# Kernel tuning notes

Hardware: AMD Instinct MI355X
Metric: run time of the kernel (lower is better)

The kernel has to match this reference:

```python
import jax, jax.numpy as jnp
import numpy as np

B, N, E, S, ANN_D, N_STEPS = 16384, 70, 3, 10, 1, 5


def setup_inputs() -> dict:
    key = jax.random.key(0)
    ks = jax.random.split(key, 10)
    std = 0.02
    annotation = jax.random.normal(ks[0], (B, N), jnp.float32)
    A_raw = jax.random.uniform(ks[1], (N, N * E), jnp.float32) + 1e-3
    A = A_raw / A_raw.sum(axis=1, keepdims=True)  # row-normalized like torch.div(A, sum(A,1))
    W_in = jax.random.normal(ks[2], (E, S, S), jnp.float32) * std
    b_in = jnp.zeros((E, S), jnp.float32)
    Wr = jax.random.normal(ks[3], (S, 2 * S), jnp.float32) * std
    br = jnp.zeros((S,), jnp.float32)
    Wz = jax.random.normal(ks[4], (S, 2 * S), jnp.float32) * std
    bz = jnp.zeros((S,), jnp.float32)
    Wh = jax.random.normal(ks[5], (S, 2 * S), jnp.float32) * std
    bh = jnp.zeros((S,), jnp.float32)
    Wo1 = jax.random.normal(ks[6], (S, S + ANN_D), jnp.float32) * std
    bo1 = jnp.zeros((S,), jnp.float32)
    Wo2 = jax.random.normal(ks[7], (1, S), jnp.float32) * std
    bo2 = jnp.zeros((1,), jnp.float32)
    return {"annotation": annotation, "A": A, "W_in": W_in, "b_in": b_in,
            "Wr": Wr, "br": br, "Wz": Wz, "bz": bz, "Wh": Wh, "bh": bh,
            "Wo1": Wo1, "bo1": bo1, "Wo2": Wo2, "bo2": bo2}


def reference(annotation, A, W_in, b_in, Wr, br, Wz, bz, Wh, bh, Wo1, bo1, Wo2, bo2):
    b, n = annotation.shape
    ann = annotation[..., None]  # [B, N, 1]
    # initial state: annotation padded with zeros to state_dim
    prop = jnp.concatenate([ann, jnp.zeros((b, n, S - ANN_D), annotation.dtype)], axis=2)  # [B,N,S]
    for _ in range(N_STEPS):
        # per-edge-type linear: [B,E,N,S]; view order is edge-type-major (matches torch stack/transpose/view)
        ins = jnp.einsum('bnd,efd->benf', prop, W_in) + b_in[None, :, None, :]
        ins = ins.reshape(b, E * n, S)  # [B, E*N, S]
        a_in = jnp.einsum('nm,bms->bns', A, ins)  # bmm aggregation, [B,N,S]
        a = jnp.concatenate([a_in, prop], axis=2)  # [B,N,2S]
        r = jax.nn.sigmoid(a @ Wr.T + br)
        z = jax.nn.sigmoid(a @ Wz.T + bz)
        joined = jnp.concatenate([a_in, r * prop], axis=2)
        h_hat = jnp.tanh(joined @ Wh.T + bh)
        prop = (1.0 - z) * prop + z * h_hat
    join_state = jnp.concatenate([prop, ann], axis=2)  # [B,N,S+1]
    out = jnp.tanh(join_state @ Wo1.T + bo1) @ Wo2.T + bo2  # [B,N,1]
    return out.sum(axis=2)  # [B,N]
```

## Files before the change

### kernel.cpp

```cpp
#include <hip/hip_runtime.h>
#include <hip/hip_bf16.h>

typedef _Float16 v8h __attribute__((ext_vector_type(8)));
typedef _Float16 v4h __attribute__((ext_vector_type(4)));
typedef _Float16 v2h __attribute__((ext_vector_type(2)));
typedef float    v4f __attribute__((ext_vector_type(4)));

#define NTOT  16384
#define NN    70
#define STEPS 5
#define TPB   64
#define NBLK  NTOT
#define CATN  40
#define CATH  3208
#define USTR  232
#define UH    (10*USTR)

#define PWO1 0
#define PWO2 120
#define PBO2 130
#define NWP  132

#define OFR  1024
#define OFZ  1536
#define OFH  2048
#define OFA  2560
#define NWF  20480
#define PREPB 40

__device__ __align__(16) float    g_w[NWP];
__device__ __align__(16) _Float16 g_wf[NWF];
__device__ int g_flag;

__device__ __forceinline__ float fast_sigmoid(float x) {
    return __builtin_amdgcn_rcpf(1.0f + __expf(-x));
}
__device__ __forceinline__ float fast_tanh(float x) {
    float ax = fabsf(x);
    float e  = __expf(-2.0f * ax);
    float t  = (1.0f - e) * __builtin_amdgcn_rcpf(1.0f + e);
    return copysignf(t, x);
}

struct __align__(16) Smem {
    _Float16 U[UH];
    _Float16 cat[CATH];
};

__global__ void prep_kernel(const void* annv, const void* Av,
    const void* winv, const void* binv, const void* wrv, const void* brv,
    const void* wzv, const void* bzv, const void* whv, const void* bhv,
    const void* wo1v, const void* bo1v, const void* wo2v, const void* bo2v)
{
    __shared__ int sflag;
    if (threadIdx.x == 0) {
        const unsigned short* u = (const unsigned short*)annv;
        int good = 0;
        for (int k = 0; k < 128; ++k) {
            unsigned short bb = u[k];
            int ex = (bb >> 7) & 0xFF;
            if (bb == 0 || (ex >= 101 && ex <= 131)) ++good;
        }
        sflag = (good >= 112) ? 1 : 0;
        if (blockIdx.x == 0) g_flag = sflag;
    }
    __syncthreads();
    const int f = sflag;
    #define RD(p, i) (f ? (float)((const __hip_bfloat16*)(p))[i] : ((const float*)(p))[i])
    const int tid = threadIdx.x;
    if (blockIdx.x == 0) {
        for (int idx = tid; idx < 120; idx += blockDim.x) {
            const int s = idx / 12, cc = idx - s*12;
            g_w[PWO1 + idx] = (cc < 11) ? RD(wo1v, s*11 + cc) : RD(bo1v, s);
        }
        for (int idx = tid; idx < 10; idx += blockDim.x) g_w[PWO2 + idx] = RD(wo2v, idx);
        if (tid == 0) { g_w[PBO2] = RD(bo2v, 0); g_w[PBO2+1] = 0.f; }
    }
    for (int idx = blockIdx.x*blockDim.x + tid; idx < NWF; idx += gridDim.x*blockDim.x) {
        float val = 0.f;
        if (idx < OFR) {
            const int nt = idx >> 9, rem = idx & 511, lane = rem >> 3, j = rem & 7;
            const int k = ((lane >> 4) << 3) + j, col = nt*16 + (lane & 15);
            if (col < 30) {
                const int e = col / 10, s = col - e*10;
                if (k >= 16 && k < 26) val = RD(winv, e*100 + s*10 + (k-16));
                else if (k == 26)      val = RD(binv, e*10 + s);
            }
        } else if (idx < OFH) {
            const int i2 = idx - OFR;
            const int mt = i2 >> 9, rem = i2 & 511, lane = rem >> 3, j = rem & 7;
            const int k = ((lane >> 4) << 3) + j, s = lane & 15;
            if (s < 10) {
                const void* Wv = mt ? wzv : wrv;
                const void* bv = mt ? bzv : brv;
                if (k < 10)                 val = RD(Wv, s*20 + k);
                else if (k >= 16 && k < 26) val = RD(Wv, s*20 + 10 + (k-16));
                else if (k == 26)           val = RD(bv, s);
            }
        } else if (idx < OFA) {
            const int i2 = idx - OFH;
            const int lane = i2 >> 3, j = i2 & 7;
            const int k = ((lane >> 4) << 3) + j, s = lane & 15;
            if (s < 10) {
                if (k < 10)                 val = RD(whv, s*20 + k);
                else if (k >= 16 && k < 26) val = RD(whv, s*20 + 10 + (k-16));
                else if (k == 26)           val = RD(bhv, s);
            }
        } else {
            const int i2 = idx - OFA;
            const int w = i2 / 3584, rem = i2 - w*3584;
            const int kt = rem >> 9, r2 = rem & 511, lane = r2 >> 3, j = r2 & 7;
            const int m = w*16 + (lane & 15);
            const int k = kt*32 + ((lane >> 4) << 3) + j;
            const int e = k / 72, mm = k - e*72;
            if (m < NN && e < 3 && mm < NN) val = RD(Av, m*210 + e*70 + mm);
        }
        g_wf[idx] = (_Float16)val;
    }
    #undef RD
}

template<typename T>
__device__ __forceinline__ void run_impl(const void* annv, void* outv, Smem& sm)
{
    const T* ann_g = (const T*)annv;
    T* out_g       = (T*)outv;
    const int lane = threadIdx.x;
    const int blk  = blockIdx.x;
    const int q    = lane >> 4;
    const int c    = lane & 15;
    const float* __restrict__ gw = g_w;

    {
        const int4 zz = {0,0,0,0};
        int4* z = (int4*)&sm;
        #pragma unroll 4
        for (int i = lane; i < (int)(sizeof(Smem)/16); i += TPB) z[i] = zz;
    }
    __syncthreads();

    for (int n2 = lane; n2 < NN; n2 += TPB) {
        sm.cat[n2*CATN + 16] = (_Float16)(float)ann_g[blk*NN + n2];
        sm.cat[n2*CATN + 26] = (_Float16)1.0f;
    }
    __syncthreads();

    #define PHASE1() do {                                                        \
        const v8h w1f0 = *(const v8h*)&g_wf[      lane*8];                       \
        const v8h w1f1 = *(const v8h*)&g_wf[512 + lane*8];                       \
        _Pragma("unroll")                                                        \
        for (int mt = 0; mt < 5; ++mt) {                                         \
            const v8h af = *(const v8h*)&sm.cat[(mt*16 + c)*CATN + q*8];         \
            const int node0 = mt*16 + q*4;                                       \
            _Pragma("unroll")                                                    \
            for (int nt = 0; nt < 2; ++nt) {                                     \
                v4f acc = {0.f,0.f,0.f,0.f};                                     \
                acc = __builtin_amdgcn_mfma_f32_16x16x32_f16(                    \
                        af, nt ? w1f1 : w1f0, acc, 0,0,0);                       \
                const int colw = nt*16 + c;                                      \
                if (colw < 30 && node0 <= 68) {                                  \
                    const int e = colw / 10, s = colw - e*10;                    \
                    v4h hv = {(_Float16)acc[0],(_Float16)acc[1],                 \
                              (_Float16)acc[2],(_Float16)acc[3]};                \
                    *(v4h*)&sm.U[s*USTR + e*72 + node0] = hv;                    \
                }                                                                \
            }                                                                    \
        }                                                                        \
    } while(0)

    PHASE1();
    __syncthreads();

    #pragma unroll 1
    for (int step = 0; step < STEPS; ++step) {
        {
            v8h bfr[7];
            #pragma unroll
            for (int kt = 0; kt < 7; ++kt)
                bfr[kt] = *(const v8h*)&sm.U[c*USTR + q*8 + kt*32];
            #pragma unroll
            for (int mt = 0; mt < 5; ++mt) {
                v4f acc = {0.f,0.f,0.f,0.f};
                #pragma unroll
                for (int kt = 0; kt < 7; ++kt)
                    acc = __builtin_amdgcn_mfma_f32_16x16x32_f16(
                        bfr[kt],
                        *(const v8h*)&g_wf[OFA + (mt*7+kt)*512 + lane*8],
                        acc, 0,0,0);
                const int node = mt*16 + c;
                if (node < NN) {
                    const v4h hv = {(_Float16)acc[0],(_Float16)acc[1],
                                    (_Float16)acc[2],(_Float16)acc[3]};
                    _Float16* wp = &sm.cat[node*CATN + q*4];
                    if (q < 2)       *(v4h*)wp = hv;
                    else if (q == 2) *(v2h*)wp = (v2h){hv[0], hv[1]};
                }
            }
        }
        __syncthreads();

        v4h zgp[5], pgp[5];
        {
            const v8h wrf = *(const v8h*)&g_wf[OFR + lane*8];
            const v8h wzf = *(const v8h*)&g_wf[OFZ + lane*8];
            #pragma unroll
            for (int nt = 0; nt < 5; ++nt) {
                const int node = nt*16 + c;
                const v8h bf = *(const v8h*)&sm.cat[node*CATN + q*8];
                v4f ar = {0.f,0.f,0.f,0.f}, az = {0.f,0.f,0.f,0.f};
                ar = __builtin_amdgcn_mfma_f32_16x16x32_f16(wrf, bf, ar, 0,0,0);
                az = __builtin_amdgcn_mfma_f32_16x16x32_f16(wzf, bf, az, 0,0,0);
                const v4h pv = *(const v4h*)&sm.cat[node*CATN + 16 + q*4];
                v4h rp, zh;
                #pragma unroll
                for (int i = 0; i < 4; ++i) {
                    const float p = (float)pv[i];
                    zh[i] = (_Float16)fast_sigmoid(az[i]);
                    rp[i] = (_Float16)(fast_sigmoid(ar[i]) * p);
                }
                zgp[nt] = zh; pgp[nt] = pv;
                if (node < NN) {
                    _Float16* wp = &sm.cat[node*CATN + 16 + q*4];
                    if (q < 2)       *(v4h*)wp = rp;
                    else if (q == 2) *(v2h*)wp = (v2h){rp[0], rp[1]};
                }
            }
        }
        __syncthreads();

        {
            const v8h whf = *(const v8h*)&g_wf[OFH + lane*8];
            #pragma unroll
            for (int nt = 0; nt < 5; ++nt) {
                const int node = nt*16 + c;
                const v8h bf2 = *(const v8h*)&sm.cat[node*CATN + q*8];
                v4f ah = {0.f,0.f,0.f,0.f};
                ah = __builtin_amdgcn_mfma_f32_16x16x32_f16(whf, bf2, ah, 0,0,0);
                v4h pn;
                #pragma unroll
                for (int i = 0; i < 4; ++i) {
                    const float hh = fast_tanh(ah[i]);
                    const float p  = (float)pgp[nt][i];
                    const float z  = (float)zgp[nt][i];
                    pn[i] = (_Float16)(p + z*(hh - p));
                }
                if (node < NN) {
                    _Float16* wp = &sm.cat[node*CATN + 16 + q*4];
                    if (q < 2)       *(v4h*)wp = pn;
                    else if (q == 2) *(v2h*)wp = (v2h){pn[0], pn[1]};
                }
            }
        }
        __syncthreads();

        if (step < STEPS-1) {
            PHASE1();
            __syncthreads();
        }
    }
    #undef PHASE1

    for (int n2 = lane; n2 < NN; n2 += TPB) {
        const _Float16* pc = &sm.cat[n2*CATN + 16];
        const v8h p8 = *(const v8h*)pc;
        const v2h p2 = *(const v2h*)(pc + 8);
        float pr[10];
        #pragma unroll
        for (int i = 0; i < 8; ++i) pr[i] = (float)p8[i];
        pr[8] = (float)p2[0]; pr[9] = (float)p2[1];
        const float av = (float)ann_g[blk*NN + n2];
        float o = gw[PBO2];
        #pragma unroll
        for (int s = 0; s < 10; ++s) {
            const float* wr_ = &gw[PWO1 + s*12];
            float acc = wr_[11] + wr_[10]*av;
            #pragma unroll
            for (int d = 0; d < 10; ++d) acc += pr[d]*wr_[d];
            o += fast_tanh(acc) * gw[PWO2 + s];
        }
        out_g[blk*NN + n2] = (T)o;
    }
}

__global__ __launch_bounds__(TPB, 2)
void ggnn_kernel(const void* annv, void* outv)
{
    __shared__ Smem sm;
    if (g_flag)
        run_impl<__hip_bfloat16>(annv, outv, sm);
    else
        run_impl<float>(annv, outv, sm);
}

extern "C" void kernel_launch(void* const* d_in, const int* in_sizes, int n_in,
                              void* d_out, int out_size, void* d_ws, size_t ws_size,
                              hipStream_t stream) {
    (void)in_sizes; (void)n_in; (void)out_size; (void)d_ws; (void)ws_size;
    hipLaunchKernelGGL(prep_kernel, dim3(PREPB), dim3(256), 0, stream,
        d_in[0], d_in[1], d_in[2], d_in[3], d_in[4], d_in[5], d_in[6],
        d_in[7], d_in[8], d_in[9], d_in[10], d_in[11], d_in[12], d_in[13]);
    hipLaunchKernelGGL(ggnn_kernel, dim3(NBLK), dim3(TPB), 0, stream,
        d_in[0], d_out);
}
```

Baseline: 290.1 us.

## Swizzle concat tile layout and double-buffer adjacency fragment loads

Shrinks the per-node concat row stride from 40 to 32 halves and applies an XOR swizzle on the 8-element chunk index, so the vector LDS accesses avoid bank conflicts while using less shared memory. The aggregation MFMA loop now preloads the adjacency weight fragments for two row tiles into registers and alternates between two buffers, with scheduling barriers, so global loads overlap the MFMA chains. This raises register pressure and adds address arithmetic on every shared-memory access.

After: 299.7 us. 1.03x slower.

```diff
diff --git a/kernel.cpp b/kernel.cpp
--- a/kernel.cpp
+++ b/kernel.cpp
@@ -11,8 +11,8 @@
 #define STEPS 5
 #define TPB   64
 #define NBLK  NTOT
-#define CATN  40
-#define CATH  3208
+#define CATN  32
+#define CATH  (80*CATN)
 #define USTR  232
 #define UH    (10*USTR)
 
@@ -40,6 +40,11 @@
     float e  = __expf(-2.0f * ax);
     float t  = (1.0f - e) * __builtin_amdgcn_rcpf(1.0f + e);
     return copysignf(t, x);
+}
+
+__device__ __forceinline__ int cat_off(int node, int k) {
+    const int sw = (node ^ (node >> 2)) & 3;
+    return node*CATN + (((k >> 3) ^ sw) << 3) + (k & 7);
 }
 
 struct __align__(16) Smem {
@@ -140,8 +145,8 @@
     __syncthreads();
 
     for (int n2 = lane; n2 < NN; n2 += TPB) {
-        sm.cat[n2*CATN + 16] = (_Float16)(float)ann_g[blk*NN + n2];
-        sm.cat[n2*CATN + 26] = (_Float16)1.0f;
+        sm.cat[cat_off(n2, 16)] = (_Float16)(float)ann_g[blk*NN + n2];
+        sm.cat[cat_off(n2, 26)] = (_Float16)1.0f;
     }
     __syncthreads();
 
@@ -150,7 +155,7 @@
         const v8h w1f1 = *(const v8h*)&g_wf[512 + lane*8];                       \
         _Pragma("unroll")                                                        \
         for (int mt = 0; mt < 5; ++mt) {                                         \
-            const v8h af = *(const v8h*)&sm.cat[(mt*16 + c)*CATN + q*8];         \
+            const v8h af = *(const v8h*)&sm.cat[cat_off(mt*16 + c, q*8)];        \
             const int node0 = mt*16 + q*4;                                       \
             _Pragma("unroll")                                                    \
             for (int nt = 0; nt < 2; ++nt) {                                     \
@@ -174,28 +179,68 @@
     #pragma unroll 1
     for (int step = 0; step < STEPS; ++step) {
         {
+            const _Float16* adjb = &g_wf[OFA + lane*8];
+            v8h pa[7], pb[7];
+            #pragma unroll
+            for (int kt = 0; kt < 7; ++kt) pa[kt] = *(const v8h*)(adjb + (0*7+kt)*512);
+            #pragma unroll
+            for (int kt = 0; kt < 7; ++kt) pb[kt] = *(const v8h*)(adjb + (1*7+kt)*512);
             v8h bfr[7];
             #pragma unroll
             for (int kt = 0; kt < 7; ++kt)
                 bfr[kt] = *(const v8h*)&sm.U[c*USTR + q*8 + kt*32];
-            #pragma unroll
-            for (int mt = 0; mt < 5; ++mt) {
-                v4f acc = {0.f,0.f,0.f,0.f};
-                #pragma unroll
-                for (int kt = 0; kt < 7; ++kt)
-                    acc = __builtin_amdgcn_mfma_f32_16x16x32_f16(
-                        bfr[kt],
-                        *(const v8h*)&g_wf[OFA + (mt*7+kt)*512 + lane*8],
-                        acc, 0,0,0);
-                const int node = mt*16 + c;
-                if (node < NN) {
-                    const v4h hv = {(_Float16)acc[0],(_Float16)acc[1],
-                                    (_Float16)acc[2],(_Float16)acc[3]};
-                    _Float16* wp = &sm.cat[node*CATN + q*4];
-                    if (q < 2)       *(v4h*)wp = hv;
-                    else if (q == 2) *(v2h*)wp = (v2h){hv[0], hv[1]};
-                }
-            }
+
+            #define P2_STORE(mtt, acc) do {                                      \
+                const int node = (mtt)*16 + c;                                   \
+                if (node < NN) {                                                 \
+                    const v4h hv = {(_Float16)acc[0],(_Float16)acc[1],           \
+                                    (_Float16)acc[2],(_Float16)acc[3]};          \
+                    if (q < 2)       *(v4h*)&sm.cat[cat_off(node, q*4)] = hv;    \
+                    else if (q == 2) *(v2h*)&sm.cat[cat_off(node, 8)]            \
+                                         = (v2h){hv[0], hv[1]};                  \
+                } } while(0)
+
+            { v4f acc = {0.f,0.f,0.f,0.f};
+              #pragma unroll
+              for (int kt = 0; kt < 7; ++kt)
+                  acc = __builtin_amdgcn_mfma_f32_16x16x32_f16(bfr[kt], pa[kt], acc, 0,0,0);
+              P2_STORE(0, acc);
+              __builtin_amdgcn_sched_barrier(0);
+              #pragma unroll
+              for (int kt = 0; kt < 7; ++kt) pa[kt] = *(const v8h*)(adjb + (2*7+kt)*512);
+            }
+            { v4f acc = {0.f,0.f,0.f,0.f};
+              #pragma unroll
+              for (int kt = 0; kt < 7; ++kt)
+                  acc = __builtin_amdgcn_mfma_f32_16x16x32_f16(bfr[kt], pb[kt], acc, 0,0,0);
+              P2_STORE(1, acc);
+              __builtin_amdgcn_sched_barrier(0);
+              #pragma unroll
+              for (int kt = 0; kt < 7; ++kt) pb[kt] = *(const v8h*)(adjb + (3*7+kt)*512);
+            }
+            { v4f acc = {0.f,0.f,0.f,0.f};
+              #pragma unroll
+              for (int kt = 0; kt < 7; ++kt)
+                  acc = __builtin_amdgcn_mfma_f32_16x16x32_f16(bfr[kt], pa[kt], acc, 0,0,0);
+              P2_STORE(2, acc);
+              __builtin_amdgcn_sched_barrier(0);
+              #pragma unroll
+              for (int kt = 0; kt < 7; ++kt) pa[kt] = *(const v8h*)(adjb + (4*7+kt)*512);
+            }
+            { v4f acc = {0.f,0.f,0.f,0.f};
+              #pragma unroll
+              for (int kt = 0; kt < 7; ++kt)
+                  acc = __builtin_amdgcn_mfma_f32_16x16x32_f16(bfr[kt], pb[kt], acc, 0,0,0);
+              P2_STORE(3, acc);
+              __builtin_amdgcn_sched_barrier(0);
+            }
+            { v4f acc = {0.f,0.f,0.f,0.f};
+              #pragma unroll
+              for (int kt = 0; kt < 7; ++kt)
+                  acc = __builtin_amdgcn_mfma_f32_16x16x32_f16(bfr[kt], pa[kt], acc, 0,0,0);
+              P2_STORE(4, acc);
+            }
+            #undef P2_STORE
         }
         __syncthreads();
 
@@ -206,11 +251,11 @@
             #pragma unroll
             for (int nt = 0; nt < 5; ++nt) {
                 const int node = nt*16 + c;
-                const v8h bf = *(const v8h*)&sm.cat[node*CATN + q*8];
+                const v8h bf = *(const v8h*)&sm.cat[cat_off(node, q*8)];
                 v4f ar = {0.f,0.f,0.f,0.f}, az = {0.f,0.f,0.f,0.f};
                 ar = __builtin_amdgcn_mfma_f32_16x16x32_f16(wrf, bf, ar, 0,0,0);
                 az = __builtin_amdgcn_mfma_f32_16x16x32_f16(wzf, bf, az, 0,0,0);
-                const v4h pv = *(const v4h*)&sm.cat[node*CATN + 16 + q*4];
+                const v4h pv = *(const v4h*)&sm.cat[cat_off(node, 16 + q*4)];
                 v4h rp, zh;
                 #pragma unroll
                 for (int i = 0; i < 4; ++i) {
@@ -220,9 +265,8 @@
                 }
                 zgp[nt] = zh; pgp[nt] = pv;
                 if (node < NN) {
-                    _Float16* wp = &sm.cat[node*CATN + 16 + q*4];
-                    if (q < 2)       *(v4h*)wp = rp;
-                    else if (q == 2) *(v2h*)wp = (v2h){rp[0], rp[1]};
+                    if (q < 2)       *(v4h*)&sm.cat[cat_off(node, 16 + q*4)] = rp;
+                    else if (q == 2) *(v2h*)&sm.cat[cat_off(node, 24)] = (v2h){rp[0], rp[1]};
                 }
             }
         }
@@ -233,7 +277,7 @@
             #pragma unroll
             for (int nt = 0; nt < 5; ++nt) {
                 const int node = nt*16 + c;
-                const v8h bf2 = *(const v8h*)&sm.cat[node*CATN + q*8];
+                const v8h bf2 = *(const v8h*)&sm.cat[cat_off(node, q*8)];
                 v4f ah = {0.f,0.f,0.f,0.f};
                 ah = __builtin_amdgcn_mfma_f32_16x16x32_f16(whf, bf2, ah, 0,0,0);
                 v4h pn;
@@ -245,9 +289,8 @@
                     pn[i] = (_Float16)(p + z*(hh - p));
                 }
                 if (node < NN) {
-                    _Float16* wp = &sm.cat[node*CATN + 16 + q*4];
-                    if (q < 2)       *(v4h*)wp = pn;
-                    else if (q == 2) *(v2h*)wp = (v2h){pn[0], pn[1]};
+                    if (q < 2)       *(v4h*)&sm.cat[cat_off(node, 16 + q*4)] = pn;
+                    else if (q == 2) *(v2h*)&sm.cat[cat_off(node, 24)] = (v2h){pn[0], pn[1]};
                 }
             }
         }
@@ -261,9 +304,8 @@
     #undef PHASE1
 
     for (int n2 = lane; n2 < NN; n2 += TPB) {
-        const _Float16* pc = &sm.cat[n2*CATN + 16];
-        const v8h p8 = *(const v8h*)pc;
-        const v2h p2 = *(const v2h*)(pc + 8);
+        const v8h p8 = *(const v8h*)&sm.cat[cat_off(n2, 16)];
+        const v2h p2 = *(const v2h*)&sm.cat[cat_off(n2, 24)];
         float pr[10];
         #pragma unroll
         for (int i = 0; i < 8; ++i) pr[i] = (float)p8[i];
```
